# Optimization experiments

Measured on AMD Instinct MI355X. Metric: run time of the kernel, lower is better.

## Reference

```python
import jax, jax.numpy as jnp
import numpy as np

B, T, D = 32, 1024, 512

def _xavier(key, shape):
    fan_in, fan_out = shape[1], shape[0]
    bound = float(np.sqrt(6.0 / (fan_in + fan_out)))
    return jax.random.uniform(key, shape, jnp.float32, -bound, bound)

def setup_inputs() -> dict:
    key = jax.random.key(0)
    ks = jax.random.split(key, 10)
    lin_bound = float(1.0 / np.sqrt(D))
    def lin(kw, kb):
        W = jax.random.uniform(kw, (D, D), jnp.float32, -lin_bound, lin_bound)
        b = jax.random.uniform(kb, (D,), jnp.float32, -lin_bound, lin_bound)
        return W, b
    Wk_w, Wk_b = lin(ks[0], ks[1])
    Wv_w, Wv_b = lin(ks[2], ks[3])
    Wq_w, Wq_b = lin(ks[4], ks[5])
    Wo_w, Wo_b = lin(ks[6], ks[7])
    w = _xavier(ks[8], (T, T))
    x = jax.random.normal(ks[9], (B, T, D), jnp.float32)
    return {"x": x, "Wk_w": Wk_w, "Wk_b": Wk_b, "Wv_w": Wv_w, "Wv_b": Wv_b,
            "Wq_w": Wq_w, "Wq_b": Wq_b, "w": w, "Wo_w": Wo_w, "Wo_b": Wo_b}

def reference(x, Wk_w, Wk_b, Wv_w, Wv_b, Wq_w, Wq_b, w, Wo_w, Wo_b):
    # K, V, Q: [B, T, D]  (torch Linear: x @ W.T + b)
    K = jnp.einsum('btd,ed->bte', x, Wk_w) + Wk_b
    V = jnp.einsum('btd,ed->bte', x, Wv_w) + Wv_b
    # exp_w: [T, T], row-wise max-stabilized position bias
    exp_w = jnp.exp(w - jnp.max(w, axis=-1, keepdims=True))
    # Faithful to original: max over dim=0 (batch dim) of K
    exp_K = jnp.exp(K - jnp.max(K, axis=0, keepdims=True))  # [B, T, D]
    num = jnp.einsum('ts,bsd->btd', exp_w, exp_K * V)
    den = jnp.einsum('ts,bsd->btd', exp_w, exp_K)
    Yt = num / den
    Q = jnp.einsum('btd,ed->bte', x, Wq_w) + Wq_b
    Yt = jax.nn.sigmoid(Q) * Yt
    out = jnp.einsum('btd,ed->bte', Yt, Wo_w) + Wo_b
    return out
```

## Files before the change

### kernel.cpp

```cpp
#include <hip/hip_runtime.h>
#include <stdint.h>

typedef unsigned short u16;
typedef __attribute__((ext_vector_type(4))) float f32x4;
typedef __attribute__((ext_vector_type(8))) __bf16 bf16x8;

__device__ __forceinline__ float b2f(u16 u) {
  union { unsigned int i; float f; } v; v.i = ((unsigned int)u) << 16; return v.f;
}
__device__ __forceinline__ u16 f2b(float f) {
  union { float f; unsigned int i; } v; v.f = f;
  unsigned int x = v.i;
  return (u16)((x + 0x7fffu + ((x >> 16) & 1u)) >> 16);
}

__device__ __forceinline__ void async_ld16(const u16* g, u16* l) {
  __builtin_amdgcn_global_load_lds((const __attribute__((address_space(1))) void*)g,
                                   (__attribute__((address_space(3))) void*)l, 16, 0, 0);
}

__global__ void detect_kernel(const u16* __restrict__ x, int* __restrict__ flag)
{
  const int tid = threadIdx.x;
  int found = 0;
  for (int i = tid; i < 32768; i += 256) {
    u16 u = x[i];
    if ((u & 0x7F80u) == 0x7F80u) found = 1;
  }
  unsigned long long m = __ballot(found != 0);
  __shared__ int sf[4];
  if ((tid & 63) == 0) sf[tid >> 6] = (m != 0ULL) ? 1 : 0;
  __syncthreads();
  if (tid == 0) flag[0] = (sf[0] | sf[1] | sf[2] | sf[3]);
}

__global__ __launch_bounds__(256)
void conv_kernel(const void* __restrict__ in, u16* __restrict__ out, long n,
                 const int* __restrict__ flag)
{
  const long i = ((long)blockIdx.x * 256 + threadIdx.x) * 8;
  if (i >= n) return;
  if (flag[0]) {
    const float* p = (const float*)in + i;
    u16 o[8];
#pragma unroll
    for (int j = 0; j < 8; j++) o[j] = f2b(p[j]);
    *(uint4*)(out + i) = *(const uint4*)o;
  } else {
    *(uint4*)(out + i) = *(const uint4*)((const u16*)in + i);
  }
}

#define BM 128
#define BN 128
#define BK 32

template<int EPI>
__global__ __launch_bounds__(256)
void gemm_bt(const u16* __restrict__ A, const u16* __restrict__ B,
             const void* __restrict__ bias, void* __restrict__ Cv,
             const int* __restrict__ flag,
             int M, int N, int K, long strideC)
{
  __shared__ __align__(16) u16 sA[BM * BK];
  __shared__ __align__(16) u16 sB[BN * BK];

  const int tid  = threadIdx.x;
  const int lane = tid & 63;
  const int wv   = tid >> 6;
  const int fl = flag[0];
  u16* Cb16 = (u16*)Cv;

  const int m0 = blockIdx.x * BM;
  const int n0 = blockIdx.y * BN;

  const int ldRow = wv * 32;
  const int lr = lane >> 2;
  const int lc = lane & 3;
  const u16* gA = A + (long)(m0 + ldRow + lr) * K + lc * 8;
  const u16* gB = B + (long)(n0 + ldRow + lr) * K + lc * 8;
  u16* lA0 = sA + (ldRow + lr) * BK + lc * 8;
  u16* lA1 = sA + (ldRow + 16 + lr) * BK + lc * 8;
  u16* lB0 = sB + (ldRow + lr) * BK + lc * 8;
  u16* lB1 = sB + (ldRow + 16 + lr) * BK + lc * 8;

  f32x4 acc[4][4];
#pragma unroll
  for (int i = 0; i < 4; i++)
#pragma unroll
    for (int j = 0; j < 4; j++) acc[i][j] = (f32x4)0.0f;

  const int waveM = (wv >> 1) * 64;
  const int waveN = (wv & 1) * 64;
  const int quad  = lane >> 4;
  const int ll    = lane & 15;

  for (int k0 = 0; k0 < K; k0 += BK) {
    async_ld16(gA,          lA0);
    async_ld16(gA + 16 * K, lA1);
    async_ld16(gB,          lB0);
    async_ld16(gB + 16 * K, lB1);
    gA += BK; gB += BK;
    __syncthreads();

    bf16x8 aF[4], bF[4];
#pragma unroll
    for (int i = 0; i < 4; i++) {
      aF[i] = *(const bf16x8*)(sA + (waveM + i * 16 + ll) * BK + quad * 8);
      bF[i] = *(const bf16x8*)(sB + (waveN + i * 16 + ll) * BK + quad * 8);
    }
#pragma unroll
    for (int i = 0; i < 4; i++)
#pragma unroll
      for (int j = 0; j < 4; j++)
        acc[i][j] = __builtin_amdgcn_mfma_f32_16x16x32_bf16(aF[i], bF[j], acc[i][j], 0, 0, 0);
    __syncthreads();
  }

#pragma unroll
  for (int i = 0; i < 4; i++) {
    const int rowb = m0 + waveM + i * 16 + quad * 4;
#pragma unroll
    for (int j = 0; j < 4; j++) {
      const int col = n0 + waveN + j * 16 + ll;
      const float bv = fl ? ((const float*)bias)[col] : b2f(((const u16*)bias)[col]);
#pragma unroll
      for (int r = 0; r < 4; r++) {
        const long idx = (long)(rowb + r) * N + col;
        const float v = acc[i][j][r] + bv;
        if (EPI == 0) {
          Cb16[idx] = f2b(v);
        } else {
          const long g = strideC + idx;
          if (fl) ((float*)Cv)[g] = v;
          else    ((u16*)Cv)[g]   = f2b(v);
        }
      }
    }
  }
}

__global__ __launch_bounds__(256)
void gemm_proj3(const u16* __restrict__ A, const u16* __restrict__ Bw,
                const void* __restrict__ kb, const void* __restrict__ vb,
                const void* __restrict__ qb,
                u16* __restrict__ Kp, u16* __restrict__ Vp, u16* __restrict__ Qp,
                const int* __restrict__ flag, int M)
{
  const int KD = 512;
  __shared__ __align__(16) u16 sA[BM * BK];
  __shared__ __align__(16) u16 sB[BN * BK];

  const int tid  = threadIdx.x;
  const int lane = tid & 63;
  const int wv   = tid >> 6;
  const int fl = flag[0];

  const int m0 = blockIdx.x * BM;
  const int n0 = blockIdx.y * BN;

  const int ldRow = wv * 32;
  const int lr = lane >> 2;
  const int lc = lane & 3;
  const u16* gA = A  + (long)(m0 + ldRow + lr) * KD + lc * 8;
  const u16* gB = Bw + (long)(n0 + ldRow + lr) * KD + lc * 8;
  u16* lA0 = sA + (ldRow + lr) * BK + lc * 8;
  u16* lA1 = sA + (ldRow + 16 + lr) * BK + lc * 8;
  u16* lB0 = sB + (ldRow + lr) * BK + lc * 8;
  u16* lB1 = sB + (ldRow + 16 + lr) * BK + lc * 8;

  f32x4 acc[4][4];
#pragma unroll
  for (int i = 0; i < 4; i++)
#pragma unroll
    for (int j = 0; j < 4; j++) acc[i][j] = (f32x4)0.0f;

  const int waveM = (wv >> 1) * 64;
  const int waveN = (wv & 1) * 64;
  const int quad  = lane >> 4;
  const int ll    = lane & 15;

  for (int k0 = 0; k0 < KD; k0 += BK) {
    async_ld16(gA,           lA0);
    async_ld16(gA + 16 * KD, lA1);
    async_ld16(gB,           lB0);
    async_ld16(gB + 16 * KD, lB1);
    gA += BK; gB += BK;
    __syncthreads();

    bf16x8 aF[4], bF[4];
#pragma unroll
    for (int i = 0; i < 4; i++) {
      aF[i] = *(const bf16x8*)(sA + (waveM + i * 16 + ll) * BK + quad * 8);
      bF[i] = *(const bf16x8*)(sB + (waveN + i * 16 + ll) * BK + quad * 8);
    }
#pragma unroll
    for (int i = 0; i < 4; i++)
#pragma unroll
      for (int j = 0; j < 4; j++)
        acc[i][j] = __builtin_amdgcn_mfma_f32_16x16x32_bf16(aF[i], bF[j], acc[i][j], 0, 0, 0);
    __syncthreads();
  }

#pragma unroll
  for (int i = 0; i < 4; i++) {
    const int rowb = m0 + waveM + i * 16 + quad * 4;
#pragma unroll
    for (int j = 0; j < 4; j++) {
      const int col = n0 + waveN + j * 16 + ll;
      const int sel = col >> 9;
      const int cs  = col & 511;
      const void* bp = (sel == 0) ? kb : (sel == 1) ? vb : qb;
      u16* dst = (sel == 0) ? Kp : (sel == 1) ? Vp : Qp;
      const float bv = fl ? ((const float*)bp)[cs] : b2f(((const u16*)bp)[cs]);
#pragma unroll
      for (int r = 0; r < 4; r++)
        dst[(long)(rowb + r) * 512 + cs] = f2b(acc[i][j][r] + bv);
    }
  }
}

#define AM 128
#define AN 64
#define ABK 32

__global__ __launch_bounds__(256, 2)
void gemm_aft(const u16* __restrict__ ew, const u16* __restrict__ Pt,
              const u16* __restrict__ PVt, const u16* __restrict__ Q,
              u16* __restrict__ Yt)
{
  const int T = 1024, D = 512;
  __shared__ __align__(16) u16 sA[AM * ABK];
  __shared__ __align__(16) u16 sB[AN * ABK];
  __shared__ __align__(16) u16 sC[AN * ABK];

  const int tid  = threadIdx.x;
  const int lane = tid & 63;
  const int wv   = tid >> 6;
  const int b    = blockIdx.z;

  const u16* Ptb  = Pt  + (long)b * D * T;
  const u16* PVtb = PVt + (long)b * D * T;
  const u16* Qb   = Q   + (long)b * T * D;
  u16*       Ytb  = Yt  + (long)b * T * D;

  const int m0 = blockIdx.x * AM;
  const int n0 = blockIdx.y * AN;

  const int ldRow = wv * 16;
  const int lr = lane >> 2;
  const int lc = lane & 3;
  const u16* gA = ew   + (long)(m0 + ldRow + lr) * T + lc * 8;
  const u16* gB = Ptb  + (long)(n0 + ldRow + lr) * T + lc * 8;
  const u16* gC = PVtb + (long)(n0 + ldRow + lr) * T + lc * 8;
  u16* lA0 = sA + (ldRow + lr) * ABK + lc * 8;
  u16* lA1 = sA + (64 + ldRow + lr) * ABK + lc * 8;
  u16* lB0 = sB + (ldRow + lr) * ABK + lc * 8;
  u16* lC0 = sC + (ldRow + lr) * ABK + lc * 8;

  f32x4 accN[4][2], accD[4][2];
#pragma unroll
  for (int i = 0; i < 4; i++)
#pragma unroll
    for (int j = 0; j < 2; j++) { accN[i][j] = (f32x4)0.0f; accD[i][j] = (f32x4)0.0f; }

  const int waveM = (wv >> 1) * 64;
  const int waveN = (wv & 1) * 32;
  const int quad  = lane >> 4;
  const int ll    = lane & 15;

  for (int k0 = 0; k0 < T; k0 += ABK) {
    async_ld16(gA,          lA0);
    async_ld16(gA + 64 * T, lA1);
    async_ld16(gB,          lB0);
    async_ld16(gC,          lC0);
    gA += ABK; gB += ABK; gC += ABK;
    __syncthreads();

    bf16x8 aF[4], bF[2], cF[2];
#pragma unroll
    for (int i = 0; i < 4; i++)
      aF[i] = *(const bf16x8*)(sA + (waveM + i * 16 + ll) * ABK + quad * 8);
#pragma unroll
    for (int j = 0; j < 2; j++) {
      bF[j] = *(const bf16x8*)(sB + (waveN + j * 16 + ll) * ABK + quad * 8);
      cF[j] = *(const bf16x8*)(sC + (waveN + j * 16 + ll) * ABK + quad * 8);
    }
#pragma unroll
    for (int i = 0; i < 4; i++)
#pragma unroll
      for (int j = 0; j < 2; j++) {
        accD[i][j] = __builtin_amdgcn_mfma_f32_16x16x32_bf16(aF[i], bF[j], accD[i][j], 0, 0, 0);
        accN[i][j] = __builtin_amdgcn_mfma_f32_16x16x32_bf16(aF[i], cF[j], accN[i][j], 0, 0, 0);
      }
    __syncthreads();
  }

#pragma unroll
  for (int i = 0; i < 4; i++) {
    const int rowb = m0 + waveM + i * 16 + quad * 4;
#pragma unroll
    for (int j = 0; j < 2; j++) {
      const int col = n0 + waveN + j * 16 + ll;
#pragma unroll
      for (int r = 0; r < 4; r++) {
        const long idx = (long)(rowb + r) * D + col;
        const float q  = b2f(Qb[idx]);
        const float t  = __expf(-q);
        const float rc = __builtin_amdgcn_rcpf(accD[i][j][r] * (1.0f + t));
        Ytb[idx] = f2b(accN[i][j][r] * rc);
      }
    }
  }
}

__global__ __launch_bounds__(256)
void expw_kernel(const void* __restrict__ w, u16* __restrict__ ew,
                 const int* __restrict__ flag)
{
  const int fl = flag[0];
  const int t = blockIdx.x;
  const int tid = threadIdx.x;
  float v[4];
  float m = -1e30f;
#pragma unroll
  for (int i = 0; i < 4; i++) {
    const long idx = (long)t * 1024 + tid + i * 256;
    float val = fl ? ((const float*)w)[idx] : b2f(((const u16*)w)[idx]);
    v[i] = val; m = fmaxf(m, val);
  }
#pragma unroll
  for (int off = 32; off > 0; off >>= 1) m = fmaxf(m, __shfl_xor(m, off, 64));
  __shared__ float sm[4];
  if ((tid & 63) == 0) sm[tid >> 6] = m;
  __syncthreads();
  m = fmaxf(fmaxf(sm[0], sm[1]), fmaxf(sm[2], sm[3]));
  u16* orow = ew + (long)t * 1024;
#pragma unroll
  for (int i = 0; i < 4; i++) orow[tid + i * 256] = f2b(__expf(v[i] - m));
}

__global__ __launch_bounds__(256)
void kmax_kernel(const u16* __restrict__ K, u16* __restrict__ Km)
{
  const long TD = 1024L * 512;
  const long base = ((long)blockIdx.x * 256 + threadIdx.x) * 8;
  float m[8];
#pragma unroll
  for (int j = 0; j < 8; j++) m[j] = -1e30f;
  for (int b = 0; b < 32; b++) {
    uint4 u = *(const uint4*)(K + b * TD + base);
    const u16* p = (const u16*)&u;
#pragma unroll
    for (int j = 0; j < 8; j++) m[j] = fmaxf(m[j], b2f(p[j]));
  }
  u16 outv[8];
#pragma unroll
  for (int j = 0; j < 8; j++) outv[j] = f2b(m[j]);
  *(uint4*)(Km + base) = *(const uint4*)outv;
}

__global__ __launch_bounds__(256)
void pexp_kernel(const u16* __restrict__ K, const u16* __restrict__ V,
                 const u16* __restrict__ Km,
                 u16* __restrict__ Pt, u16* __restrict__ PVt)
{
  const int T = 1024, D = 512;
  const long TD = (long)T * D;
  const int s0 = blockIdx.x * 64;
  const int d0 = blockIdx.y * 64;
  const int b  = blockIdx.z;
  __shared__ u16 lp[64 * 66];
  __shared__ u16 lpv[64 * 66];
  const int tid  = threadIdx.x;
  const int srow = tid >> 3;
  const int c8   = (tid & 7) * 8;

#pragma unroll
  for (int h = 0; h < 2; h++) {
    const int s = srow + h * 32;
    const long gidx = (long)b * TD + (long)(s0 + s) * D + d0 + c8;
    uint4 ku = *(const uint4*)(K + gidx);
    uint4 vu = *(const uint4*)(V + gidx);
    uint4 mu = *(const uint4*)(Km + (long)(s0 + s) * D + d0 + c8);
    const u16* kp = (const u16*)&ku;
    const u16* vp = (const u16*)&vu;
    const u16* mp = (const u16*)&mu;
#pragma unroll
    for (int j = 0; j < 8; j++) {
      float p  = __expf(b2f(kp[j]) - b2f(mp[j]));
      float pv = p * b2f(vp[j]);
      lp[s * 66 + c8 + j]  = f2b(p);
      lpv[s * 66 + c8 + j] = f2b(pv);
    }
  }
  __syncthreads();

  const int lane = tid & 63;
  const int wv   = tid >> 6;
#pragma unroll
  for (int it = 0; it < 16; it++) {
    const int d = wv * 16 + it;
    const long oidx = (long)b * TD + (long)(d0 + d) * T + s0 + lane;
    Pt[oidx]  = lp[lane * 66 + d];
    PVt[oidx] = lpv[lane * 66 + d];
  }
}

extern "C" void kernel_launch(void* const* d_in, const int* in_sizes, int n_in,
                              void* d_out, int out_size, void* d_ws, size_t ws_size,
                              hipStream_t stream)
{
  const int B = 32, T = 1024, D = 512;
  const long TD = (long)T * D;
  const void* x    = d_in[0];
  const void* Wk_w = d_in[1];
  const void* Wk_b = d_in[2];
  const void* Wv_w = d_in[3];
  const void* Wv_b = d_in[4];
  const void* Wq_w = d_in[5];
  const void* Wq_b = d_in[6];
  const void* w    = d_in[7];
  const void* Wo_w = d_in[8];
  const void* Wo_b = d_in[9];

  char* ws = (char*)d_ws;
  const size_t MB = 1024 * 1024;
  u16* xb    = (u16*)(ws + 0);
  u16* Kbuf  = (u16*)(ws + 32 * MB);
  u16* ewb   = (u16*)(ws + 64 * MB);
  u16* kmb   = (u16*)(ws + 66 * MB);
  u16* Wpack = (u16*)(ws + 67 * MB);
  u16* Wvb   = Wpack + 512 * 512;
  u16* Wqb   = Wpack + 2 * 512 * 512;
  u16* Wob   = (u16*)(ws + 68 * MB + 512 * 1024);
  int* flag  = (int*)(ws + 69 * MB);
  u16* Ytb   = Kbuf;

  dim3 blk(256);

  detect_kernel<<<dim3(1), blk, 0, stream>>>((const u16*)x, flag);
  conv_kernel<<<dim3(8192), blk, 0, stream>>>(x,    xb,    (long)B * T * D, flag);
  conv_kernel<<<dim3(128),  blk, 0, stream>>>(Wk_w, Wpack, (long)D * D, flag);
  conv_kernel<<<dim3(128),  blk, 0, stream>>>(Wv_w, Wvb,   (long)D * D, flag);
  conv_kernel<<<dim3(128),  blk, 0, stream>>>(Wq_w, Wqb,   (long)D * D, flag);
  conv_kernel<<<dim3(128),  blk, 0, stream>>>(Wo_w, Wob,   (long)D * D, flag);
  expw_kernel<<<dim3(1024), blk, 0, stream>>>(w, ewb, flag);

  if (ws_size >= 200 * MB) {
    u16* Vb   = (u16*)(ws + 70 * MB);
    u16* Qb   = (u16*)(ws + 102 * MB);
    u16* Ptb  = (u16*)(ws + 134 * MB);
    u16* PVtb = (u16*)(ws + 166 * MB);

    gemm_proj3<<<dim3((B * T) / 128, 12), blk, 0, stream>>>(
        xb, Wpack, Wk_b, Wv_b, Wq_b, Kbuf, Vb, Qb, flag, B * T);

    kmax_kernel<<<dim3(256), blk, 0, stream>>>(Kbuf, kmb);
    pexp_kernel<<<dim3(16, 8, 32), blk, 0, stream>>>(Kbuf, Vb, kmb, Ptb, PVtb);

    gemm_aft<<<dim3(T / AM, D / AN, 32), blk, 0, stream>>>(ewb, Ptb, PVtb, Qb, Ytb);

    gemm_bt<3><<<dim3((B * T) / 128, D / 128), blk, 0, stream>>>(
        Ytb, Wob, Wo_b, d_out, flag, B * T, D, D, 0);
  } else {
    const int NB = 4, NC = B / NB;
    char* ck = ws + 70 * MB;
    const size_t cb = (size_t)NB * TD * sizeof(u16);
    u16* Vc   = (u16*)(ck);
    u16* Ptc  = (u16*)(ck + cb);
    u16* PVtc = (u16*)(ck + 2 * cb);
    u16* Qc   = (u16*)(ck + 3 * cb);
    u16* Ytc  = Vc;

    gemm_bt<0><<<dim3((B * T) / 128, D / 128), blk, 0, stream>>>(
        xb, Wpack, Wk_b, Kbuf, flag, B * T, D, D, 0);
    kmax_kernel<<<dim3(256), blk, 0, stream>>>(Kbuf, kmb);

    dim3 gP((NB * T) / 128, D / 128, 1);
    dim3 gA(T / AM, D / AN, NB);
    for (int c = 0; c < NC; c++) {
      const long off = (long)c * NB * TD;
      gemm_bt<0><<<gP, blk, 0, stream>>>(xb + off, Wvb, Wv_b, Vc, flag, NB * T, D, D, 0);
      gemm_bt<0><<<gP, blk, 0, stream>>>(xb + off, Wqb, Wq_b, Qc, flag, NB * T, D, D, 0);
      pexp_kernel<<<dim3(16, 8, NB), blk, 0, stream>>>(Kbuf + off, Vc, kmb, Ptc, PVtc);
      gemm_aft<<<gA, blk, 0, stream>>>(ewb, Ptc, PVtc, Qc, Ytc);
      gemm_bt<3><<<gP, blk, 0, stream>>>(Ytc, Wob, Wo_b, d_out, flag, NB * T, D, D, off);
    }
  }
}
```

Measured before the change: 407.7 us.

## Swizzle LDS tile layout and remap blocks across XCDs for L2 locality

Applies an XOR swizzle to the column chunk on both the global-to-LDS async loads and the LDS fragment reads, to avoid bank conflicts when MFMA fragments are read from shared memory. It also remaps block indices so that consecutive tiles land on the same XCD, improving L2 reuse of shared A/B panels in all three GEMM kernels. The aft kernel remap hardcodes grid dims of 8x8 in x/y, which adds fragility if the grid shape changes.

```diff
diff --git a/kernel.cpp b/kernel.cpp
--- a/kernel.cpp
+++ b/kernel.cpp
@@ -71,14 +71,27 @@
   const int fl = flag[0];
   u16* Cb16 = (u16*)Cv;
 
-  const int m0 = blockIdx.x * BM;
-  const int n0 = blockIdx.y * BN;
+  int bx = blockIdx.x, by = blockIdx.y;
+  {
+    const int nx = gridDim.x, ny = gridDim.y;
+    if ((nx & 7) == 0) {
+      const int d   = bx + nx * by;
+      const int xcd = d & 7;
+      const int s   = d >> 3;
+      const int q   = s / ny;
+      bx = xcd * (nx >> 3) + q;
+      by = s - q * ny;
+    }
+  }
+  const int m0 = bx * BM;
+  const int n0 = by * BN;
 
   const int ldRow = wv * 32;
   const int lr = lane >> 2;
   const int lc = lane & 3;
-  const u16* gA = A + (long)(m0 + ldRow + lr) * K + lc * 8;
-  const u16* gB = B + (long)(n0 + ldRow + lr) * K + lc * 8;
+  const int scol = (lc ^ ((lr >> 1) & 3)) * 8;
+  const u16* gA = A + (long)(m0 + ldRow + lr) * K + scol;
+  const u16* gB = B + (long)(n0 + ldRow + lr) * K + scol;
   u16* lA0 = sA + (ldRow + lr) * BK + lc * 8;
   u16* lA1 = sA + (ldRow + 16 + lr) * BK + lc * 8;
   u16* lB0 = sB + (ldRow + lr) * BK + lc * 8;
@@ -94,6 +107,7 @@
   const int waveN = (wv & 1) * 64;
   const int quad  = lane >> 4;
   const int ll    = lane & 15;
+  const int rs    = (quad ^ ((ll >> 1) & 3)) * 8;
 
   for (int k0 = 0; k0 < K; k0 += BK) {
     async_ld16(gA,          lA0);
@@ -106,8 +120,8 @@
     bf16x8 aF[4], bF[4];
 #pragma unroll
     for (int i = 0; i < 4; i++) {
-      aF[i] = *(const bf16x8*)(sA + (waveM + i * 16 + ll) * BK + quad * 8);
-      bF[i] = *(const bf16x8*)(sB + (waveN + i * 16 + ll) * BK + quad * 8);
+      aF[i] = *(const bf16x8*)(sA + (waveM + i * 16 + ll) * BK + rs);
+      bF[i] = *(const bf16x8*)(sB + (waveN + i * 16 + ll) * BK + rs);
     }
 #pragma unroll
     for (int i = 0; i < 4; i++)
@@ -156,14 +170,27 @@
   const int wv   = tid >> 6;
   const int fl = flag[0];
 
-  const int m0 = blockIdx.x * BM;
-  const int n0 = blockIdx.y * BN;
+  int bx = blockIdx.x, by = blockIdx.y;
+  {
+    const int nx = gridDim.x, ny = gridDim.y;
+    if ((nx & 7) == 0) {
+      const int d   = bx + nx * by;
+      const int xcd = d & 7;
+      const int s   = d >> 3;
+      const int q   = s / ny;
+      bx = xcd * (nx >> 3) + q;
+      by = s - q * ny;
+    }
+  }
+  const int m0 = bx * BM;
+  const int n0 = by * BN;
 
   const int ldRow = wv * 32;
   const int lr = lane >> 2;
   const int lc = lane & 3;
-  const u16* gA = A  + (long)(m0 + ldRow + lr) * KD + lc * 8;
-  const u16* gB = Bw + (long)(n0 + ldRow + lr) * KD + lc * 8;
+  const int scol = (lc ^ ((lr >> 1) & 3)) * 8;
+  const u16* gA = A  + (long)(m0 + ldRow + lr) * KD + scol;
+  const u16* gB = Bw + (long)(n0 + ldRow + lr) * KD + scol;
   u16* lA0 = sA + (ldRow + lr) * BK + lc * 8;
   u16* lA1 = sA + (ldRow + 16 + lr) * BK + lc * 8;
   u16* lB0 = sB + (ldRow + lr) * BK + lc * 8;
@@ -179,6 +206,7 @@
   const int waveN = (wv & 1) * 64;
   const int quad  = lane >> 4;
   const int ll    = lane & 15;
+  const int rs    = (quad ^ ((ll >> 1) & 3)) * 8;
 
   for (int k0 = 0; k0 < KD; k0 += BK) {
     async_ld16(gA,           lA0);
@@ -191,8 +219,8 @@
     bf16x8 aF[4], bF[4];
 #pragma unroll
     for (int i = 0; i < 4; i++) {
-      aF[i] = *(const bf16x8*)(sA + (waveM + i * 16 + ll) * BK + quad * 8);
-      bF[i] = *(const bf16x8*)(sB + (waveN + i * 16 + ll) * BK + quad * 8);
+      aF[i] = *(const bf16x8*)(sA + (waveM + i * 16 + ll) * BK + rs);
+      bF[i] = *(const bf16x8*)(sB + (waveN + i * 16 + ll) * BK + rs);
     }
 #pragma unroll
     for (int i = 0; i < 4; i++)
@@ -237,22 +265,35 @@
   const int tid  = threadIdx.x;
   const int lane = tid & 63;
   const int wv   = tid >> 6;
-  const int b    = blockIdx.z;
+
+  int xt = blockIdx.x, yt = blockIdx.y, zt = blockIdx.z;
+  {
+    const int nz = gridDim.z;
+    const int d   = xt + (yt << 3) + (zt << 6);
+    const int xcd = d & 7;
+    const int s   = d >> 3;
+    const int panel = xcd * nz + (s >> 3);
+    xt = s & 7;
+    yt = panel & 7;
+    zt = panel >> 3;
+  }
+  const int b = zt;
 
   const u16* Ptb  = Pt  + (long)b * D * T;
   const u16* PVtb = PVt + (long)b * D * T;
   const u16* Qb   = Q   + (long)b * T * D;
   u16*       Ytb  = Yt  + (long)b * T * D;
 
-  const int m0 = blockIdx.x * AM;
-  const int n0 = blockIdx.y * AN;
+  const int m0 = xt * AM;
+  const int n0 = yt * AN;
 
   const int ldRow = wv * 16;
   const int lr = lane >> 2;
   const int lc = lane & 3;
-  const u16* gA = ew   + (long)(m0 + ldRow + lr) * T + lc * 8;
-  const u16* gB = Ptb  + (long)(n0 + ldRow + lr) * T + lc * 8;
-  const u16* gC = PVtb + (long)(n0 + ldRow + lr) * T + lc * 8;
+  const int scol = (lc ^ ((lr >> 1) & 3)) * 8;
+  const u16* gA = ew   + (long)(m0 + ldRow + lr) * T + scol;
+  const u16* gB = Ptb  + (long)(n0 + ldRow + lr) * T + scol;
+  const u16* gC = PVtb + (long)(n0 + ldRow + lr) * T + scol;
   u16* lA0 = sA + (ldRow + lr) * ABK + lc * 8;
   u16* lA1 = sA + (64 + ldRow + lr) * ABK + lc * 8;
   u16* lB0 = sB + (ldRow + lr) * ABK + lc * 8;
@@ -268,6 +309,7 @@
   const int waveN = (wv & 1) * 32;
   const int quad  = lane >> 4;
   const int ll    = lane & 15;
+  const int rs    = (quad ^ ((ll >> 1) & 3)) * 8;
 
   for (int k0 = 0; k0 < T; k0 += ABK) {
     async_ld16(gA,          lA0);
@@ -280,11 +322,11 @@
     bf16x8 aF[4], bF[2], cF[2];
 #pragma unroll
     for (int i = 0; i < 4; i++)
-      aF[i] = *(const bf16x8*)(sA + (waveM + i * 16 + ll) * ABK + quad * 8);
+      aF[i] = *(const bf16x8*)(sA + (waveM + i * 16 + ll) * ABK + rs);
 #pragma unroll
     for (int j = 0; j < 2; j++) {
-      bF[j] = *(const bf16x8*)(sB + (waveN + j * 16 + ll) * ABK + quad * 8);
-      cF[j] = *(const bf16x8*)(sC + (waveN + j * 16 + ll) * ABK + quad * 8);
+      bF[j] = *(const bf16x8*)(sB + (waveN + j * 16 + ll) * ABK + rs);
+      cF[j] = *(const bf16x8*)(sC + (waveN + j * 16 + ll) * ABK + rs);
     }
 #pragma unroll
     for (int i = 0; i < 4; i++)
```

Result: faster. 383.5 us (-5.9%).
